# Optimization experiments

Hardware: AMD Instinct MI355X
Metric: run time of the kernel (lower is better)

Reference implementation:

```python
import jax, jax.numpy as jnp
import numpy as np

B, S, HID = 2, 2048, 2048
NH, NKV = 32, 8
HD = HID // NH          # 64
G = NH // NKV           # 4 query heads per kv head
ROPE_BASE = 10000.0


def _rope_cos_sin(seq_len, head_dim, dtype):
    inv_freq = 1.0 / (ROPE_BASE ** (jnp.arange(0, head_dim, 2, dtype=jnp.float32) / head_dim))
    freqs = jnp.arange(seq_len, dtype=jnp.float32)[:, None] * inv_freq[None, :]  # [S, HD/2]
    cos = jnp.cos(freqs)
    sin = jnp.sin(freqs)
    # torch code does cos.repeat(1, 2): tile along last dim -> [S, HD]
    cos = jnp.concatenate([cos, cos], axis=-1).astype(dtype)
    sin = jnp.concatenate([sin, sin], axis=-1).astype(dtype)
    return cos, sin


def _rotate_half(x):
    x1, x2 = jnp.split(x, 2, axis=-1)
    return jnp.concatenate([-x2, x1], axis=-1)


def setup_inputs() -> dict:
    key = jax.random.key(0)
    ks = jax.random.split(key, 5)
    sc = 0.02
    return {
        "hidden_states": jax.random.normal(ks[0], (B, S, HID), dtype=jnp.float32),
        "wq": jax.random.normal(ks[1], (HID, HID), dtype=jnp.float32) * sc,
        "wk": jax.random.normal(ks[2], (NKV * HD, HID), dtype=jnp.float32) * sc,
        "wv": jax.random.normal(ks[3], (NKV * HD, HID), dtype=jnp.float32) * sc,
        "wo": jax.random.normal(ks[4], (HID, HID), dtype=jnp.float32) * sc,
    }


def reference(hidden_states, wq, wk, wv, wo):
    b, s, _ = hidden_states.shape
    # projections (torch Linear: y = x @ W^T)
    q = (hidden_states @ wq.T).reshape(b, s, NH, HD).transpose(0, 2, 1, 3)   # [B,NH,S,HD]
    k = (hidden_states @ wk.T).reshape(b, s, NKV, HD).transpose(0, 2, 1, 3)  # [B,NKV,S,HD]
    v = (hidden_states @ wv.T).reshape(b, s, NKV, HD).transpose(0, 2, 1, 3)  # [B,NKV,S,HD]

    cos, sin = _rope_cos_sin(s, HD, q.dtype)  # [S,HD]
    q = q * cos + _rotate_half(q) * sin
    k = k * cos + _rotate_half(k) * sin

    # GQA: group query heads per kv head instead of repeat_interleave (same math)
    qg = q.reshape(b, NKV, G, s, HD)
    scale = HD ** -0.5
    scores = jnp.einsum('bkgsd,bktd->bkgst', qg, k) * scale     # [B,NKV,G,S,S]
    attn = jax.nn.softmax(scores, axis=-1)
    out = jnp.einsum('bkgst,bktd->bkgsd', attn, v)              # [B,NKV,G,S,HD]
    out = out.reshape(b, NH, s, HD).transpose(0, 2, 1, 3).reshape(b, s, HID)
    return out @ wo.T
```

## Files before the change

### kernel.cpp

```cpp
#include <hip/hip_runtime.h>
#include <stdint.h>

typedef __attribute__((ext_vector_type(8))) short bf16x8;
typedef __attribute__((ext_vector_type(4))) short bf16x4;
typedef __attribute__((ext_vector_type(4))) float f32x4;
typedef __attribute__((ext_vector_type(4))) unsigned u32x4;
typedef __attribute__((ext_vector_type(2))) unsigned u32x2;

#define S_LEN 2048
#define HIDDEN 2048
#define N_HEADS 32
#define N_KV 8
#define HEAD_DIM 64
#define KVD (N_KV * HEAD_DIM)

__device__ __forceinline__ float bf2f(short u) {
  return __builtin_bit_cast(float, ((unsigned)(unsigned short)u) << 16);
}
__device__ __forceinline__ short f2bf(float f) {
  unsigned u = __builtin_bit_cast(unsigned, f);
  u += 0x7FFFu + ((u >> 16) & 1u);
  return (short)(u >> 16);
}
__device__ __forceinline__ unsigned cvtpk(float lo, float hi) {
  unsigned r;
  asm("v_cvt_pk_bf16_f32 %0, %1, %2" : "=v"(r) : "v"(lo), "v"(hi));
  return r;
}
__device__ __forceinline__ bf16x8 cvt8(f32x4 lo, f32x4 hi) {
  bf16x8 r;
#pragma unroll
  for (int j = 0; j < 4; ++j) { r[j] = f2bf(lo[j]); r[j + 4] = f2bf(hi[j]); }
  return r;
}
__device__ __forceinline__ void storeC(float* p, float v) { *p = v; }
__device__ __forceinline__ void storeC(short* p, float v) { *p = f2bf(v); }

__device__ __forceinline__ void gll16(const void* g, void* l) {
  __builtin_amdgcn_global_load_lds(
      (const __attribute__((address_space(1))) void*)g,
      (__attribute__((address_space(3))) void*)l, 16, 0, 0);
}

struct CvtArgs {
  const float* src[5];
  short* dst[5];
  int cnt4[5];
};
__global__ void cvt_bf16(CvtArgs a, int total4) {
  int u = blockIdx.x * 256 + threadIdx.x;
  const int stride = gridDim.x * 256;
  for (; u < total4; u += stride) {
    int s = 0, off = u;
    while (off >= a.cnt4[s]) { off -= a.cnt4[s]; ++s; }
    f32x4 v = *(const f32x4*)(a.src[s] + (size_t)off * 4);
    bf16x4 r;
#pragma unroll
    for (int j = 0; j < 4; ++j) r[j] = f2bf(v[j]);
    *(bf16x4*)(a.dst[s] + (size_t)off * 4) = r;
  }
}

template <typename CT>
__launch_bounds__(256, 3)
__global__ void gemm_lds(const short* __restrict__ A, const short* __restrict__ W,
                         CT* __restrict__ C, int M, int N, int K) {
  __shared__ short As[128 * 32];
  __shared__ short Ws[128 * 32];
  const int tid  = threadIdx.x;
  const int lane = tid & 63;
  const int w    = tid >> 6;
  const int wm = w >> 1, wn = w & 1;
  const int lr = lane & 15, lg = lane >> 4;
  const int m0 = blockIdx.y * 128, n0 = blockIdx.x * 128;

  const size_t a0 = (size_t)(m0 + w * 16 + (lane >> 2)) * K + (lane & 3) * 8;
  const size_t a1 = a0 + (size_t)64 * K;
  const size_t b0 = (size_t)(n0 + w * 16 + (lane >> 2)) * K + (lane & 3) * 8;
  const size_t b1 = b0 + (size_t)64 * K;
  short* lA0 = &As[(w * 16) * 32];
  short* lA1 = &As[(64 + w * 16) * 32];
  short* lB0 = &Ws[(w * 16) * 32];
  short* lB1 = &Ws[(64 + w * 16) * 32];

  f32x4 acc[4][4] = {};

  for (int k0 = 0; k0 < K; k0 += 32) {
    __syncthreads();
    gll16(A + a0 + k0, lA0);
    gll16(A + a1 + k0, lA1);
    gll16(W + b0 + k0, lB0);
    gll16(W + b1 + k0, lB1);
    __syncthreads();
    bf16x8 af[4], bfr[4];
#pragma unroll
    for (int i = 0; i < 4; ++i) {
      af[i]  = *(const bf16x8*)&As[(wm * 64 + i * 16 + lr) * 32 + lg * 8];
      bfr[i] = *(const bf16x8*)&Ws[(wn * 64 + i * 16 + lr) * 32 + lg * 8];
    }
#pragma unroll
    for (int i = 0; i < 4; ++i)
#pragma unroll
      for (int j = 0; j < 4; ++j)
        acc[i][j] = __builtin_amdgcn_mfma_f32_16x16x32_bf16(af[i], bfr[j], acc[i][j], 0, 0, 0);
  }

#pragma unroll
  for (int i = 0; i < 4; ++i)
#pragma unroll
    for (int j = 0; j < 4; ++j) {
      const int row = m0 + wm * 64 + i * 16 + lg * 4;
      const int col = n0 + wn * 64 + j * 16 + lr;
#pragma unroll
      for (int r = 0; r < 4; ++r)
        storeC(&C[(size_t)(row + r) * N + col], acc[i][j][r]);
    }
}

template <typename AT, typename CT>
__launch_bounds__(256, 2)
__global__ void gemm_bt(const AT* __restrict__ A, const float* __restrict__ W,
                        CT* __restrict__ C, int M, int N, int K) {
  __shared__ short As[128][40];
  __shared__ short Ws[128][40];
  const int tid  = threadIdx.x;
  const int lane = tid & 63;
  const int wid  = tid >> 6;
  const int wm = wid >> 1, wn = wid & 1;
  const int lr = lane & 15, lg = lane >> 4;
  const int m0 = blockIdx.y * 128, n0 = blockIdx.x * 128;
  const int srow = tid >> 2;
  const int scol = (tid & 3) * 8;

  f32x4 acc[4][4] = {};
  const AT*    Ap = A + (size_t)(m0 + srow) * K + scol;
  const float* Wp = W + (size_t)(n0 + srow) * K + scol;

  for (int k0 = 0; k0 < K; k0 += 32) {
    bf16x8 a0, a1, b0, b1;
    if constexpr (sizeof(AT) == 4) {
      a0 = cvt8(*(const f32x4*)(Ap + k0), *(const f32x4*)(Ap + k0 + 4));
      a1 = cvt8(*(const f32x4*)(Ap + (size_t)64 * K + k0),
                *(const f32x4*)(Ap + (size_t)64 * K + k0 + 4));
    } else {
      a0 = *(const bf16x8*)(Ap + k0);
      a1 = *(const bf16x8*)(Ap + (size_t)64 * K + k0);
    }
    b0 = cvt8(*(const f32x4*)(Wp + k0), *(const f32x4*)(Wp + k0 + 4));
    b1 = cvt8(*(const f32x4*)(Wp + (size_t)64 * K + k0),
              *(const f32x4*)(Wp + (size_t)64 * K + k0 + 4));
    __syncthreads();
    *(bf16x8*)&As[srow][scol]      = a0;
    *(bf16x8*)&As[srow + 64][scol] = a1;
    *(bf16x8*)&Ws[srow][scol]      = b0;
    *(bf16x8*)&Ws[srow + 64][scol] = b1;
    __syncthreads();
    bf16x8 af[4], bfr[4];
#pragma unroll
    for (int i = 0; i < 4; ++i) {
      af[i]  = *(const bf16x8*)&As[wm * 64 + i * 16 + lr][lg * 8];
      bfr[i] = *(const bf16x8*)&Ws[wn * 64 + i * 16 + lr][lg * 8];
    }
#pragma unroll
    for (int i = 0; i < 4; ++i)
#pragma unroll
      for (int j = 0; j < 4; ++j)
        acc[i][j] = __builtin_amdgcn_mfma_f32_16x16x32_bf16(af[i], bfr[j], acc[i][j], 0, 0, 0);
  }
#pragma unroll
  for (int i = 0; i < 4; ++i)
#pragma unroll
    for (int j = 0; j < 4; ++j) {
      const int row = m0 + wm * 64 + i * 16 + lg * 4;
      const int col = n0 + wn * 64 + j * 16 + lr;
#pragma unroll
      for (int r = 0; r < 4; ++r)
        storeC(&C[(size_t)(row + r) * N + col], acc[i][j][r]);
    }
}

template <int NH>
__global__ void rope_kernel(short* __restrict__ buf, int rowstride, int total) {
  int idx = blockIdx.x * 256 + threadIdx.x;
  if (idx >= total) return;
  const int i   = idx & 31;
  const int hh  = (idx >> 5) % NH;
  const int row = (idx >> 5) / NH;
  const int pos = row & (S_LEN - 1);
  const float invf = exp2f(-(float)i * (13.287712379549449f / 32.0f));
  const float ang  = (float)pos * invf;
  float sn, c;
  sincosf(ang, &sn, &c);
  size_t base = (size_t)row * rowstride + hh * 64;
  float x1 = bf2f(buf[base + i]);
  float x2 = bf2f(buf[base + i + 32]);
  buf[base + i]      = f2bf(x1 * c - x2 * sn);
  buf[base + i + 32] = f2bf(x2 * c + x1 * sn);
}

__global__ void vtrans(const short* __restrict__ Vsrc, int vs, short* __restrict__ Vtp) {
  const int t = blockIdx.x, kv = blockIdx.y, b = blockIdx.z;
  __shared__ short lt[64][72];
  const int kl = threadIdx.x >> 2;
  const int dq = (threadIdx.x & 3) * 16;
  const short* src = Vsrc + (size_t)(b * S_LEN + t * 64 + kl) * vs + kv * 64 + dq;
  bf16x8 v0 = *(const bf16x8*)src;
  bf16x8 v1 = *(const bf16x8*)(src + 8);
  *(bf16x8*)&lt[kl][dq]     = v0;
  *(bf16x8*)&lt[kl][dq + 8] = v1;
  __syncthreads();
  const int d  = threadIdx.x >> 2;
  const int cb = (threadIdx.x & 3) * 16;
  const int xm = (d & 7) << 3;
  const int c0 = cb ^ xm;
  const int c1 = c0 ^ 8;
  bf16x8 o0, o1;
#pragma unroll
  for (int j = 0; j < 8; ++j) {
    const int ca = c0 + j;
    const int ka = (ca & 32) | (((ca >> 2) & 1) << 4) | (((ca >> 3) & 3) << 2) | (ca & 3);
    o0[j] = lt[ka][d];
    const int cbb = c1 + j;
    const int kb = (cbb & 32) | (((cbb >> 2) & 1) << 4) | (((cbb >> 3) & 3) << 2) | (cbb & 3);
    o1[j] = lt[kb][d];
  }
  short* dst = Vtp + (size_t)((b * N_KV + kv) * 64 + d) * S_LEN + t * 64 + cb;
  *(bf16x8*)dst       = o0;
  *(bf16x8*)(dst + 8) = o1;
}

__device__ __forceinline__ void qkt_mfma(const bf16x8 (&kf)[4][2],
                                         const bf16x8 (&qa)[2][2],
                                         f32x4 (&sf)[2][4]) {
  __builtin_amdgcn_s_setprio(1);
#pragma unroll
  for (int nf = 0; nf < 4; ++nf)
#pragma unroll
    for (int fr = 0; fr < 2; ++fr) {
      f32x4 t = {};
      t = __builtin_amdgcn_mfma_f32_16x16x32_bf16(kf[nf][0], qa[fr][0], t, 0, 0, 0);
      t = __builtin_amdgcn_mfma_f32_16x16x32_bf16(kf[nf][1], qa[fr][1], t, 0, 0, 0);
      sf[fr][nf] = t;
    }
  __builtin_amdgcn_s_setprio(0);
}

template <int KS>
__device__ __forceinline__ void load_kf(bf16x8 (&kf)[4][2], const short* kbase, int t) {
  const short* kp = kbase + (size_t)t * 64 * KS;
#pragma unroll
  for (int nf = 0; nf < 4; ++nf) {
    kf[nf][0] = *(const bf16x8*)(kp + (size_t)nf * 16 * KS);
    kf[nf][1] = *(const bf16x8*)(kp + (size_t)nf * 16 * KS + 32);
  }
}

__device__ __forceinline__ void stage_v(short* lds, const short* vtbase, int t,
                                        int w, int lane) {
  const int l3 = lane >> 3, l7 = lane & 7;
#pragma unroll
  for (int ci = 0; ci < 2; ++ci) {
    const int call = 2 * w + ci;
    const int d = call * 8 + l3;
    gll16(vtbase + (size_t)d * S_LEN + t * 64 + l7 * 8, lds + call * 512);
  }
}

__device__ __forceinline__ void load_vb(bf16x8 (&vb)[2][4], const short* lds,
                                        int lr, int lg) {
  const int xm = (lr & 7) << 3;
#pragma unroll
  for (int ks2 = 0; ks2 < 2; ++ks2)
#pragma unroll
    for (int df = 0; df < 4; ++df)
      vb[ks2][df] = *(const bf16x8*)&lds[(df * 16 + lr) * 64 + ((ks2 * 32 + lg * 8) ^ xm)];
}

__device__ __forceinline__ void softmax_pv(
    f32x4 (&sf)[2][4], const bf16x8 (&vb)[2][4], f32x4 (&o)[2][4],
    float (&mrow)[2], float (&msc)[2], float (&lsum)[2],
    float SC, float THRR) {
  bf16x8 pa[2][2];
#pragma unroll
  for (int fr = 0; fr < 2; ++fr) {
    float lmax = fmaxf(fmaxf(sf[fr][0][0], sf[fr][0][1]), fmaxf(sf[fr][0][2], sf[fr][0][3]));
#pragma unroll
    for (int nf = 1; nf < 4; ++nf) {
      float m01 = fmaxf(sf[fr][nf][0], sf[fr][nf][1]);
      float m23 = fmaxf(sf[fr][nf][2], sf[fr][nf][3]);
      lmax = fmaxf(lmax, fmaxf(m01, m23));
    }
    if (!__all(lmax <= mrow[fr] + THRR)) {
      float mx = fmaxf(lmax, __shfl_xor(lmax, 16));
      mx = fmaxf(mx, __shfl_xor(mx, 32));
      const float mnew  = fmaxf(mrow[fr], mx);
      const float alpha = __builtin_amdgcn_exp2f((mrow[fr] - mnew) * SC);
      mrow[fr] = mnew;
      msc[fr]  = mnew * SC;
      lsum[fr] *= alpha;
#pragma unroll
      for (int df = 0; df < 4; ++df) o[fr][df] *= alpha;
    }
    const float nm = msc[fr];
#pragma unroll
    for (int nf = 0; nf < 4; ++nf)
#pragma unroll
      for (int r = 0; r < 4; ++r)
        sf[fr][nf][r] = __builtin_amdgcn_exp2f(fmaf(sf[fr][nf][r], SC, -nm));
    {
      float t0 = (sf[fr][0][0] + sf[fr][0][1]) + (sf[fr][0][2] + sf[fr][0][3]);
      float t1 = (sf[fr][1][0] + sf[fr][1][1]) + (sf[fr][1][2] + sf[fr][1][3]);
      float t2 = (sf[fr][2][0] + sf[fr][2][1]) + (sf[fr][2][2] + sf[fr][2][3]);
      float t3 = (sf[fr][3][0] + sf[fr][3][1]) + (sf[fr][3][2] + sf[fr][3][3]);
      lsum[fr] += (t0 + t1) + (t2 + t3);
    }
#pragma unroll
    for (int ks2 = 0; ks2 < 2; ++ks2) {
      u32x4 pk;
      pk[0] = cvtpk(sf[fr][2 * ks2][0], sf[fr][2 * ks2][1]);
      pk[1] = cvtpk(sf[fr][2 * ks2][2], sf[fr][2 * ks2][3]);
      pk[2] = cvtpk(sf[fr][2 * ks2 + 1][0], sf[fr][2 * ks2 + 1][1]);
      pk[3] = cvtpk(sf[fr][2 * ks2 + 1][2], sf[fr][2 * ks2 + 1][3]);
      pa[fr][ks2] = __builtin_bit_cast(bf16x8, pk);
    }
  }
  __builtin_amdgcn_s_setprio(1);
#pragma unroll
  for (int ks2 = 0; ks2 < 2; ++ks2)
#pragma unroll
    for (int fr = 0; fr < 2; ++fr)
#pragma unroll
      for (int df = 0; df < 4; ++df)
        o[fr][df] = __builtin_amdgcn_mfma_f32_16x16x32_bf16(vb[ks2][df], pa[fr][ks2], o[fr][df], 0, 0, 0);
  __builtin_amdgcn_s_setprio(0);
}

#define NT (S_LEN / 64)
template <int QS, int KS, int OS>
__launch_bounds__(256, 2)
__global__ void attn_kernel(const short* __restrict__ Q, const short* __restrict__ K,
                            const short* __restrict__ Vtp, short* __restrict__ O) {
  const int qt = blockIdx.x, h = blockIdx.y, b = blockIdx.z;
  const int kv = h >> 2;
  const int tid  = threadIdx.x;
  const int lane = tid & 63, w = tid >> 6;
  const int lr = lane & 15, lg = lane >> 4;

  __shared__ short Vt[2][64 * 64];

  const int q0 = qt * 128 + w * 32;
  bf16x8 qa[2][2];
#pragma unroll
  for (int fr = 0; fr < 2; ++fr) {
    const short* qp = Q + (size_t)(b * S_LEN + q0 + fr * 16 + lr) * QS + h * HEAD_DIM + lg * 8;
    qa[fr][0] = *(const bf16x8*)qp;
    qa[fr][1] = *(const bf16x8*)(qp + 32);
  }

  f32x4 o[2][4] = {};
  float mrow[2] = {-1e30f, -1e30f};
  float msc[2]  = {-1e30f, -1e30f};
  float lsum[2] = {0.f, 0.f};

  const short* vtbase = Vtp + (size_t)((b * N_KV + kv) * 64) * S_LEN;
  const short* kbase  = K + (size_t)(b * S_LEN + lr) * KS + kv * HEAD_DIM + lg * 8;

  const float SC   = 0.125f * 1.4426950408889634f;
  const float THRR = 8.0f / SC;

  bf16x8 kf[4][2];
  bf16x8 vb[2][4];
  f32x4 sfA[2][4], sfB[2][4];
  stage_v(Vt[0], vtbase, 0, w, lane);
  load_kf<KS>(kf, kbase, 0);
  qkt_mfma(kf, qa, sfA);
  load_kf<KS>(kf, kbase, 1);
  __syncthreads();

  for (int t = 0; t < NT; t += 2) {
    load_vb(vb, Vt[0], lr, lg);
    stage_v(Vt[1], vtbase, t + 1, w, lane);
    qkt_mfma(kf, qa, sfB);
    if (t + 2 < NT) load_kf<KS>(kf, kbase, t + 2);
    softmax_pv(sfA, vb, o, mrow, msc, lsum, SC, THRR);
    __syncthreads();

    load_vb(vb, Vt[1], lr, lg);
    if (t + 2 < NT) {
      stage_v(Vt[0], vtbase, t + 2, w, lane);
      qkt_mfma(kf, qa, sfA);
      if (t + 3 < NT) load_kf<KS>(kf, kbase, t + 3);
    }
    softmax_pv(sfB, vb, o, mrow, msc, lsum, SC, THRR);
    __syncthreads();
  }

#pragma unroll
  for (int fr = 0; fr < 2; ++fr) {
    float ls = lsum[fr];
    ls += __shfl_xor(ls, 16);
    ls += __shfl_xor(ls, 32);
    const float invl = 1.0f / ls;
    const size_t orow = (size_t)(b * S_LEN + q0 + fr * 16 + lr) * OS + h * HEAD_DIM;
#pragma unroll
    for (int df = 0; df < 4; ++df) {
      u32x2 pk;
      pk[0] = cvtpk(o[fr][df][0] * invl, o[fr][df][1] * invl);
      pk[1] = cvtpk(o[fr][df][2] * invl, o[fr][df][3] * invl);
      *(u32x2*)&O[orow + df * 16 + 4 * lg] = pk;
    }
  }
}

extern "C" void kernel_launch(void* const* d_in, const int* in_sizes, int n_in,
                              void* d_out, int out_size, void* d_ws, size_t ws_size,
                              hipStream_t stream) {
  (void)in_sizes; (void)n_in; (void)out_size;
  const float* hidden = (const float*)d_in[0];
  const float* wq = (const float*)d_in[1];
  const float* wk = (const float*)d_in[2];
  const float* wv = (const float*)d_in[3];
  const float* wo = (const float*)d_in[4];
  float* out = (float*)d_out;

  const int M = 2 * S_LEN;
  const size_t nHid  = (size_t)M * HIDDEN;
  const size_t nW    = (size_t)HIDDEN * HIDDEN;
  const size_t nWkv  = (size_t)KVD * HIDDEN;
  const size_t nWcat = nW + 2 * nWkv;
  const int    NQKV  = HIDDEN + 2 * KVD;
  const size_t nQKV  = (size_t)M * NQKV;
  const size_t nVtp  = (size_t)M * KVD;

  const size_t fastElems = nHid + nWcat + nW + nQKV + nHid;
  if (ws_size >= fastElems * sizeof(short)) {
    short* hb   = (short*)d_ws;
    short* wcat = hb + nHid;
    short* wob  = wcat + nWcat;
    short* QKV  = wob + nW;
    short* AO   = QKV + nQKV;
    short* vtp  = hb;

    CvtArgs ca;
    ca.src[0] = hidden; ca.dst[0] = hb;            ca.cnt4[0] = (int)(nHid / 4);
    ca.src[1] = wq;     ca.dst[1] = wcat;          ca.cnt4[1] = (int)(nW / 4);
    ca.src[2] = wk;     ca.dst[2] = wcat + nW;     ca.cnt4[2] = (int)(nWkv / 4);
    ca.src[3] = wv;     ca.dst[3] = wcat + nW + nWkv; ca.cnt4[3] = (int)(nWkv / 4);
    ca.src[4] = wo;     ca.dst[4] = wob;           ca.cnt4[4] = (int)(nW / 4);
    const int total4 = (int)((nHid + nWcat + nW) / 4);
    cvt_bf16<<<2048, 256, 0, stream>>>(ca, total4);

    gemm_lds<short><<<dim3(NQKV / 128, 32), 256, 0, stream>>>(hb, wcat, QKV, M, NQKV, HIDDEN);
    vtrans<<<dim3(S_LEN / 64, N_KV, 2), 256, 0, stream>>>(QKV + HIDDEN + KVD, NQKV, vtp);
    const int rtot = M * 40 * 32;
    rope_kernel<40><<<(rtot + 255) / 256, 256, 0, stream>>>(QKV, NQKV, rtot);
    attn_kernel<3072, 3072, HIDDEN><<<dim3(S_LEN / 128, N_HEADS, 2), 256, 0, stream>>>(
        QKV, QKV + HIDDEN, vtp, AO);
    gemm_lds<float><<<dim3(16, 32), 256, 0, stream>>>(AO, wob, out, M, HIDDEN, HIDDEN);
  } else {
    short* Qb  = (short*)d_ws;
    short* Kb  = Qb + nHid;
    short* Vb  = Kb + nVtp;
    short* AO  = Vb + nVtp;
    short* vtp = AO + nHid;
    gemm_bt<float, short><<<dim3(16, 32), 256, 0, stream>>>(hidden, wq, Qb, M, HIDDEN, HIDDEN);
    gemm_bt<float, short><<<dim3(4, 32), 256, 0, stream>>>(hidden, wk, Kb, M, KVD, HIDDEN);
    gemm_bt<float, short><<<dim3(4, 32), 256, 0, stream>>>(hidden, wv, Vb, M, KVD, HIDDEN);
    const int rq = M * N_HEADS * 32, rk = M * N_KV * 32;
    rope_kernel<N_HEADS><<<(rq + 255) / 256, 256, 0, stream>>>(Qb, HIDDEN, rq);
    rope_kernel<N_KV><<<(rk + 255) / 256, 256, 0, stream>>>(Kb, KVD, rk);
    vtrans<<<dim3(S_LEN / 64, N_KV, 2), 256, 0, stream>>>(Vb, KVD, vtp);
    attn_kernel<HIDDEN, KVD, HIDDEN><<<dim3(S_LEN / 128, N_HEADS, 2), 256, 0, stream>>>(
        Qb, Kb, vtp, AO);
    gemm_bt<short, float><<<dim3(16, 32), 256, 0, stream>>>(AO, wo, out, M, HIDDEN, HIDDEN);
  }
}
```

Measured before the change: 283.9 us.

## Halve attention query tile per wave to raise occupancy

Each wave now handles 16 query rows instead of 32, so a block covers 64 queries and the grid doubles along the sequence. Accumulators, scores and softmax state shrink by half, and launch bounds rise to 4 blocks per CU for more waves in flight. In exchange, every K tile and V tile is loaded and staged twice as often per query, which raises memory and LDS traffic and lowers MFMA work per load.

```diff
diff --git a/kernel.cpp b/kernel.cpp
--- a/kernel.cpp
+++ b/kernel.cpp
@@ -230,18 +230,16 @@
 }
 
 __device__ __forceinline__ void qkt_mfma(const bf16x8 (&kf)[4][2],
-                                         const bf16x8 (&qa)[2][2],
-                                         f32x4 (&sf)[2][4]) {
+                                         const bf16x8 (&qa)[2],
+                                         f32x4 (&sf)[4]) {
   __builtin_amdgcn_s_setprio(1);
 #pragma unroll
-  for (int nf = 0; nf < 4; ++nf)
-#pragma unroll
-    for (int fr = 0; fr < 2; ++fr) {
-      f32x4 t = {};
-      t = __builtin_amdgcn_mfma_f32_16x16x32_bf16(kf[nf][0], qa[fr][0], t, 0, 0, 0);
-      t = __builtin_amdgcn_mfma_f32_16x16x32_bf16(kf[nf][1], qa[fr][1], t, 0, 0, 0);
-      sf[fr][nf] = t;
-    }
+  for (int nf = 0; nf < 4; ++nf) {
+    f32x4 t = {};
+    t = __builtin_amdgcn_mfma_f32_16x16x32_bf16(kf[nf][0], qa[0], t, 0, 0, 0);
+    t = __builtin_amdgcn_mfma_f32_16x16x32_bf16(kf[nf][1], qa[1], t, 0, 0, 0);
+    sf[nf] = t;
+  }
   __builtin_amdgcn_s_setprio(0);
 }
 
@@ -277,67 +275,61 @@
 }
 
 __device__ __forceinline__ void softmax_pv(
-    f32x4 (&sf)[2][4], const bf16x8 (&vb)[2][4], f32x4 (&o)[2][4],
-    float (&mrow)[2], float (&msc)[2], float (&lsum)[2],
-    float SC, float THRR) {
-  bf16x8 pa[2][2];
-#pragma unroll
-  for (int fr = 0; fr < 2; ++fr) {
-    float lmax = fmaxf(fmaxf(sf[fr][0][0], sf[fr][0][1]), fmaxf(sf[fr][0][2], sf[fr][0][3]));
-#pragma unroll
-    for (int nf = 1; nf < 4; ++nf) {
-      float m01 = fmaxf(sf[fr][nf][0], sf[fr][nf][1]);
-      float m23 = fmaxf(sf[fr][nf][2], sf[fr][nf][3]);
-      lmax = fmaxf(lmax, fmaxf(m01, m23));
-    }
-    if (!__all(lmax <= mrow[fr] + THRR)) {
-      float mx = fmaxf(lmax, __shfl_xor(lmax, 16));
-      mx = fmaxf(mx, __shfl_xor(mx, 32));
-      const float mnew  = fmaxf(mrow[fr], mx);
-      const float alpha = __builtin_amdgcn_exp2f((mrow[fr] - mnew) * SC);
-      mrow[fr] = mnew;
-      msc[fr]  = mnew * SC;
-      lsum[fr] *= alpha;
-#pragma unroll
-      for (int df = 0; df < 4; ++df) o[fr][df] *= alpha;
-    }
-    const float nm = msc[fr];
-#pragma unroll
-    for (int nf = 0; nf < 4; ++nf)
-#pragma unroll
-      for (int r = 0; r < 4; ++r)
-        sf[fr][nf][r] = __builtin_amdgcn_exp2f(fmaf(sf[fr][nf][r], SC, -nm));
-    {
-      float t0 = (sf[fr][0][0] + sf[fr][0][1]) + (sf[fr][0][2] + sf[fr][0][3]);
-      float t1 = (sf[fr][1][0] + sf[fr][1][1]) + (sf[fr][1][2] + sf[fr][1][3]);
-      float t2 = (sf[fr][2][0] + sf[fr][2][1]) + (sf[fr][2][2] + sf[fr][2][3]);
-      float t3 = (sf[fr][3][0] + sf[fr][3][1]) + (sf[fr][3][2] + sf[fr][3][3]);
-      lsum[fr] += (t0 + t1) + (t2 + t3);
-    }
-#pragma unroll
-    for (int ks2 = 0; ks2 < 2; ++ks2) {
-      u32x4 pk;
-      pk[0] = cvtpk(sf[fr][2 * ks2][0], sf[fr][2 * ks2][1]);
-      pk[1] = cvtpk(sf[fr][2 * ks2][2], sf[fr][2 * ks2][3]);
-      pk[2] = cvtpk(sf[fr][2 * ks2 + 1][0], sf[fr][2 * ks2 + 1][1]);
-      pk[3] = cvtpk(sf[fr][2 * ks2 + 1][2], sf[fr][2 * ks2 + 1][3]);
-      pa[fr][ks2] = __builtin_bit_cast(bf16x8, pk);
-    }
+    f32x4 (&sf)[4], const bf16x8 (&vb)[2][4], f32x4 (&o)[4],
+    float& mrow, float& msc, float& lsum, float SC, float THRR) {
+  bf16x8 pa[2];
+  float lmax = fmaxf(fmaxf(sf[0][0], sf[0][1]), fmaxf(sf[0][2], sf[0][3]));
+#pragma unroll
+  for (int nf = 1; nf < 4; ++nf) {
+    float m01 = fmaxf(sf[nf][0], sf[nf][1]);
+    float m23 = fmaxf(sf[nf][2], sf[nf][3]);
+    lmax = fmaxf(lmax, fmaxf(m01, m23));
+  }
+  if (!__all(lmax <= mrow + THRR)) {
+    float mx = fmaxf(lmax, __shfl_xor(lmax, 16));
+    mx = fmaxf(mx, __shfl_xor(mx, 32));
+    const float mnew  = fmaxf(mrow, mx);
+    const float alpha = __builtin_amdgcn_exp2f((mrow - mnew) * SC);
+    mrow = mnew;
+    msc  = mnew * SC;
+    lsum *= alpha;
+#pragma unroll
+    for (int df = 0; df < 4; ++df) o[df] *= alpha;
+  }
+  const float nm = msc;
+#pragma unroll
+  for (int nf = 0; nf < 4; ++nf)
+#pragma unroll
+    for (int r = 0; r < 4; ++r)
+      sf[nf][r] = __builtin_amdgcn_exp2f(fmaf(sf[nf][r], SC, -nm));
+  {
+    float t0 = (sf[0][0] + sf[0][1]) + (sf[0][2] + sf[0][3]);
+    float t1 = (sf[1][0] + sf[1][1]) + (sf[1][2] + sf[1][3]);
+    float t2 = (sf[2][0] + sf[2][1]) + (sf[2][2] + sf[2][3]);
+    float t3 = (sf[3][0] + sf[3][1]) + (sf[3][2] + sf[3][3]);
+    lsum += (t0 + t1) + (t2 + t3);
+  }
+#pragma unroll
+  for (int ks2 = 0; ks2 < 2; ++ks2) {
+    u32x4 pk;
+    pk[0] = cvtpk(sf[2 * ks2][0], sf[2 * ks2][1]);
+    pk[1] = cvtpk(sf[2 * ks2][2], sf[2 * ks2][3]);
+    pk[2] = cvtpk(sf[2 * ks2 + 1][0], sf[2 * ks2 + 1][1]);
+    pk[3] = cvtpk(sf[2 * ks2 + 1][2], sf[2 * ks2 + 1][3]);
+    pa[ks2] = __builtin_bit_cast(bf16x8, pk);
   }
   __builtin_amdgcn_s_setprio(1);
 #pragma unroll
   for (int ks2 = 0; ks2 < 2; ++ks2)
 #pragma unroll
-    for (int fr = 0; fr < 2; ++fr)
-#pragma unroll
-      for (int df = 0; df < 4; ++df)
-        o[fr][df] = __builtin_amdgcn_mfma_f32_16x16x32_bf16(vb[ks2][df], pa[fr][ks2], o[fr][df], 0, 0, 0);
+    for (int df = 0; df < 4; ++df)
+      o[df] = __builtin_amdgcn_mfma_f32_16x16x32_bf16(vb[ks2][df], pa[ks2], o[df], 0, 0, 0);
   __builtin_amdgcn_s_setprio(0);
 }
 
 #define NT (S_LEN / 64)
 template <int QS, int KS, int OS>
-__launch_bounds__(256, 2)
+__launch_bounds__(256, 4)
 __global__ void attn_kernel(const short* __restrict__ Q, const short* __restrict__ K,
                             const short* __restrict__ Vtp, short* __restrict__ O) {
   const int qt = blockIdx.x, h = blockIdx.y, b = blockIdx.z;
@@ -348,19 +340,16 @@
 
   __shared__ short Vt[2][64 * 64];
 
-  const int q0 = qt * 128 + w * 32;
-  bf16x8 qa[2][2];
-#pragma unroll
-  for (int fr = 0; fr < 2; ++fr) {
-    const short* qp = Q + (size_t)(b * S_LEN + q0 + fr * 16 + lr) * QS + h * HEAD_DIM + lg * 8;
-    qa[fr][0] = *(const bf16x8*)qp;
-    qa[fr][1] = *(const bf16x8*)(qp + 32);
-  }
-
-  f32x4 o[2][4] = {};
-  float mrow[2] = {-1e30f, -1e30f};
-  float msc[2]  = {-1e30f, -1e30f};
-  float lsum[2] = {0.f, 0.f};
+  const int q0 = qt * 64 + w * 16;
+  bf16x8 qa[2];
+  {
+    const short* qp = Q + (size_t)(b * S_LEN + q0 + lr) * QS + h * HEAD_DIM + lg * 8;
+    qa[0] = *(const bf16x8*)qp;
+    qa[1] = *(const bf16x8*)(qp + 32);
+  }
+
+  f32x4 o[4] = {};
+  float mrow = -1e30f, msc = -1e30f, lsum = 0.f;
 
   const short* vtbase = Vtp + (size_t)((b * N_KV + kv) * 64) * S_LEN;
   const short* kbase  = K + (size_t)(b * S_LEN + lr) * KS + kv * HEAD_DIM + lg * 8;
@@ -370,7 +359,7 @@
 
   bf16x8 kf[4][2];
   bf16x8 vb[2][4];
-  f32x4 sfA[2][4], sfB[2][4];
+  f32x4 sfA[4], sfB[4];
   stage_v(Vt[0], vtbase, 0, w, lane);
   load_kf<KS>(kf, kbase, 0);
   qkt_mfma(kf, qa, sfA);
@@ -395,18 +384,17 @@
     __syncthreads();
   }
 
-#pragma unroll
-  for (int fr = 0; fr < 2; ++fr) {
-    float ls = lsum[fr];
+  {
+    float ls = lsum;
     ls += __shfl_xor(ls, 16);
     ls += __shfl_xor(ls, 32);
     const float invl = 1.0f / ls;
-    const size_t orow = (size_t)(b * S_LEN + q0 + fr * 16 + lr) * OS + h * HEAD_DIM;
+    const size_t orow = (size_t)(b * S_LEN + q0 + lr) * OS + h * HEAD_DIM;
 #pragma unroll
     for (int df = 0; df < 4; ++df) {
       u32x2 pk;
-      pk[0] = cvtpk(o[fr][df][0] * invl, o[fr][df][1] * invl);
-      pk[1] = cvtpk(o[fr][df][2] * invl, o[fr][df][3] * invl);
+      pk[0] = cvtpk(o[df][0] * invl, o[df][1] * invl);
+      pk[1] = cvtpk(o[df][2] * invl, o[df][3] * invl);
       *(u32x2*)&O[orow + df * 16 + 4 * lg] = pk;
     }
   }
@@ -454,7 +442,7 @@
     vtrans<<<dim3(S_LEN / 64, N_KV, 2), 256, 0, stream>>>(QKV + HIDDEN + KVD, NQKV, vtp);
     const int rtot = M * 40 * 32;
     rope_kernel<40><<<(rtot + 255) / 256, 256, 0, stream>>>(QKV, NQKV, rtot);
-    attn_kernel<3072, 3072, HIDDEN><<<dim3(S_LEN / 128, N_HEADS, 2), 256, 0, stream>>>(
+    attn_kernel<3072, 3072, HIDDEN><<<dim3(S_LEN / 64, N_HEADS, 2), 256, 0, stream>>>(
         QKV, QKV + HIDDEN, vtp, AO);
     gemm_lds<float><<<dim3(16, 32), 256, 0, stream>>>(AO, wob, out, M, HIDDEN, HIDDEN);
   } else {
@@ -470,7 +458,7 @@
     rope_kernel<N_HEADS><<<(rq + 255) / 256, 256, 0, stream>>>(Qb, HIDDEN, rq);
     rope_kernel<N_KV><<<(rk + 255) / 256, 256, 0, stream>>>(Kb, KVD, rk);
     vtrans<<<dim3(S_LEN / 64, N_KV, 2), 256, 0, stream>>>(Vb, KVD, vtp);
-    attn_kernel<HIDDEN, KVD, HIDDEN><<<dim3(S_LEN / 128, N_HEADS, 2), 256, 0, stream>>>(
+    attn_kernel<HIDDEN, KVD, HIDDEN><<<dim3(S_LEN / 64, N_HEADS, 2), 256, 0, stream>>>(
         Qb, Kb, vtp, AO);
     gemm_bt<short, float><<<dim3(16, 32), 256, 0, stream>>>(AO, wo, out, M, HIDDEN, HIDDEN);
   }
```

After: 681.9 us. +140.2%, slower.
